# Performance work log

Measured on AMD Instinct MI355X. Metric: run time of the kernel, lower is better.

Reference implementation:

```python
import jax, jax.numpy as jnp
import numpy as np

THETA = 10000.0
NUM_HEADS = 16
MAX_SEQ_LEN = 2048

def _rope_tables(d_k, max_seq_len, theta=THETA):
    dims = jnp.arange(0, d_k, 2, dtype=jnp.float32)
    freqs = 1.0 / theta ** (dims / d_k)
    t = jnp.arange(max_seq_len, dtype=jnp.float32)
    angles = jnp.outer(t, freqs)  # (max_seq_len, d_k//2)
    return jnp.cos(angles), jnp.sin(angles)

def _apply_rope(x, token_positions, cos_tab, sin_tab):
    # x: (..., seq_len, d_k)
    cos = jnp.repeat(cos_tab[token_positions], 2, axis=-1)  # (seq_len, d_k)
    sin = jnp.repeat(sin_tab[token_positions], 2, axis=-1)
    # interleaved rotate-half: (-x1, x0, -x3, x2, ...)
    xp = x.reshape(*x.shape[:-1], -1, 2)
    x_neg = jnp.stack([-xp[..., 1], xp[..., 0]], axis=-1).reshape(x.shape)
    return x * cos + x_neg * sin

def setup_inputs() -> dict:
    key = jax.random.key(0)
    ks = jax.random.split(key, 5)
    B, S, D = 4, 2048, 1024
    scale = 1.0 / np.sqrt(D)
    return {
        "x": jax.random.normal(ks[0], (B, S, D), dtype=jnp.float32),
        "q_proj": jax.random.normal(ks[1], (D, D), dtype=jnp.float32) * scale,
        "k_proj": jax.random.normal(ks[2], (D, D), dtype=jnp.float32) * scale,
        "v_proj": jax.random.normal(ks[3], (D, D), dtype=jnp.float32) * scale,
        "o_proj": jax.random.normal(ks[4], (D, D), dtype=jnp.float32) * scale,
        "token_positions": jnp.arange(S, dtype=jnp.int64),
    }

def reference(x, q_proj, k_proj, v_proj, o_proj, token_positions):
    B, S, D = x.shape
    H = NUM_HEADS
    d_k = D // H
    cos_tab, sin_tab = _rope_tables(d_k, MAX_SEQ_LEN)

    q = (x @ q_proj).reshape(B, S, H, d_k).transpose(0, 2, 1, 3)  # (B,H,S,d_k)
    k = (x @ k_proj).reshape(B, S, H, d_k).transpose(0, 2, 1, 3)
    v = (x @ v_proj).reshape(B, S, H, d_k).transpose(0, 2, 1, 3)

    q = _apply_rope(q, token_positions, cos_tab, sin_tab)
    k = _apply_rope(k, token_positions, cos_tab, sin_tab)

    scores = jnp.einsum('bhqd,bhkd->bhqk', q, k) / jnp.sqrt(jnp.float32(d_k))
    causal = jnp.tril(jnp.ones((S, S), dtype=bool))
    scores = jnp.where(causal, scores, -jnp.inf)
    attn = jax.nn.softmax(scores, axis=-1)
    out = jnp.einsum('bhqk,bhkd->bhqd', attn, v)  # (B,H,S,d_k)
    out = out.transpose(0, 2, 1, 3).reshape(B, S, D)
    return out @ o_proj
```

## Files before the change

### kernel.cpp

```cpp
#include <hip/hip_runtime.h>
#include <hip/hip_bf16.h>
#include <stdint.h>


typedef __attribute__((ext_vector_type(8))) short short8;
typedef __attribute__((ext_vector_type(4))) float floatx4;
typedef __attribute__((ext_vector_type(16))) float floatx16;

#define MFMA16(a,b,c) __builtin_amdgcn_mfma_f32_16x16x32_bf16((a),(b),(c),0,0,0)
#define MFMA32(a,b,c) __builtin_amdgcn_mfma_f32_32x32x16_bf16((a),(b),(c),0,0,0)
#define BAR() __builtin_amdgcn_s_barrier()
#define LGKM0 asm volatile("s_waitcnt lgkmcnt(0)" ::: "memory")
#define VMCNT6 asm volatile("s_waitcnt vmcnt(6)" ::: "memory")
#define VMCNT8 asm volatile("s_waitcnt vmcnt(8)" ::: "memory")

__device__ __forceinline__ uint32_t fbits(float f){ uint32_t u; __builtin_memcpy(&u,&f,4); return u; }
__device__ __forceinline__ unsigned short f2bf(float f) {
    uint32_t u = fbits(f);
    return (unsigned short)((u + 0x7fffu + ((u>>16)&1u)) >> 16);
}
__device__ __forceinline__ float bf2f(unsigned short s){ uint32_t u = (uint32_t)s<<16; float f; __builtin_memcpy(&f,&u,4); return f; }
__device__ __forceinline__ uint32_t pkbf(float lo, float hi) {
#if __has_builtin(__builtin_amdgcn_cvt_pk_bf16_f32)
    auto r = __builtin_amdgcn_cvt_pk_bf16_f32(lo, hi);
    uint32_t u; __builtin_memcpy(&u, &r, sizeof(u));
    return u;
#else
    return __builtin_amdgcn_perm(fbits(hi)+0x8000u, fbits(lo)+0x8000u, 0x07060302u);
#endif
}
__device__ __forceinline__ float fexp2(float x) {
#if __has_builtin(__builtin_amdgcn_exp2f)
    return __builtin_amdgcn_exp2f(x);
#else
    return exp2f(x);
#endif
}

__device__ __forceinline__ void load_lds16(const unsigned short* g, unsigned short* l) {
    __builtin_amdgcn_global_load_lds(
        (const __attribute__((address_space(1))) void*)g,
        (__attribute__((address_space(3))) void*)l, 16, 0, 0);
}

__device__ __forceinline__ bool sniff_f32(const unsigned short* xr) {
    int lane = threadIdx.x & 63;
    int bad = 0;
#pragma unroll
    for (int i = 0; i < 16; i++) {
        float v = bf2f(xr[lane * 16 + i]);
        if (!(__builtin_fabsf(v) < 1e10f)) bad = 1;
    }
    return __ballot(bad != 0) != 0ull;
}

__global__ __launch_bounds__(256) void prep_k(
    const void* __restrict__ x,
    const void* __restrict__ wq, const void* __restrict__ wk,
    const void* __restrict__ wv, const void* __restrict__ wo,
    unsigned short* __restrict__ WT, unsigned short* __restrict__ WoT,
    float2* __restrict__ tab, unsigned short* __restrict__ xb) {
    int blk = blockIdx.x, t = threadIdx.x;
    bool f32 = sniff_f32((const unsigned short*)x);
    if (blk < 4096) {
        __shared__ unsigned short tile[32][33];
        int mat = blk >> 10, r = blk & 1023;
        const void* src = (mat == 0) ? wq : (mat == 1) ? wk : (mat == 2) ? wv : wo;
        unsigned short* dst = (mat < 3) ? (WT + (size_t)mat * 1048576) : WoT;
        int bx = (r & 31) * 32, by = (r >> 5) * 32;
        int tx = t & 31, ty = t >> 5;
#pragma unroll
        for (int j = 0; j < 32; j += 8) {
            size_t idx = (size_t)(by + ty + j) * 1024 + bx + tx;
            float v = f32 ? ((const float*)src)[idx] : bf2f(((const unsigned short*)src)[idx]);
            tile[ty + j][tx] = f2bf(v);
        }
        __syncthreads();
#pragma unroll
        for (int j = 0; j < 32; j += 8)
            dst[(size_t)(bx + ty + j) * 1024 + by + tx] = tile[tx][ty + j];
    } else if (blk < 4352) {
        int i = (blk - 4096) * 256 + t;
        int pos = i >> 5, j = i & 31;
        float freq = exp2f(-(float)(2 * j) * (1.0f / 64.0f) * 13.287712379549449f);
        float a = (float)pos * freq;
        tab[i] = make_float2(cosf(a), sinf(a));
    } else {
        size_t base = (size_t)(blk - 4352) * 2048 + (size_t)t * 8;
        if (f32) {
            const float4* s4 = (const float4*)((const float*)x + base);
            float4 a = s4[0], b = s4[1];
            uint4 o;
            o.x = pkbf(a.x, a.y); o.y = pkbf(a.z, a.w);
            o.z = pkbf(b.x, b.y); o.w = pkbf(b.z, b.w);
            *(uint4*)(xb + base) = o;
        } else {
            *(uint4*)(xb + base) = *(const uint4*)((const unsigned short*)x + base);
        }
    }
}

template <int MODE>
__global__ __launch_bounds__(256, 2) void gemmt(
    const unsigned short* __restrict__ A,
    const unsigned short* __restrict__ Bt,
    void* __restrict__ C0,
    unsigned short* __restrict__ C1,
    unsigned short* __restrict__ C2,
    const float2* __restrict__ tab,
    const unsigned short* __restrict__ xsniff) {
    const int K = 1024;
    extern __shared__ __align__(16) char smraw[];
    unsigned short* SL = (unsigned short*)smraw;

    int t = threadIdx.x;
    int lane = t & 63, w = t >> 6;
    int quad = lane >> 4, l15 = lane & 15;
    int wn = w * 64;

    int nbx = gridDim.x;
    int flat = blockIdx.y * nbx + blockIdx.x;
    int cpx = (nbx * gridDim.y) >> 3;
    int swzid = (flat & 7) * cpx + (flat >> 3);
    int bx = swzid % nbx, by = swzid / nbx;
    int m0 = by * 128, n0 = bx * 256;

    floatx4 acc[8][4];
#pragma unroll
    for (int i = 0; i < 8; i++)
#pragma unroll
        for (int j = 0; j < 4; j++) acc[i][j] = (floatx4){0.f, 0.f, 0.f, 0.f};

    int sg = ((t & 3) ^ ((t >> 3) & 3)) * 8;
    const unsigned short* gA = A + (size_t)(m0 + (t >> 2)) * K + sg;
    const unsigned short* gB = Bt + (size_t)(n0 + (t >> 2)) * K + sg;

    int colsw = (quad ^ ((l15 >> 1) & 3)) * 8;

#pragma unroll
    for (int kt = 0; kt < 2; kt++) {
        unsigned short* Sb = SL + kt * 12288 + w * 512;
        load_lds16(gA + kt * 32, Sb);
        load_lds16(gA + (size_t)64 * K + kt * 32, Sb + 2048);
        load_lds16(gB + kt * 32, Sb + 4096);
        load_lds16(gB + (size_t)64 * K + kt * 32, Sb + 6144);
        load_lds16(gB + (size_t)128 * K + kt * 32, Sb + 8192);
        load_lds16(gB + (size_t)192 * K + kt * 32, Sb + 10240);
    }
    VMCNT6;
    __syncthreads();

    int cur = 0, nxt = 2;
#pragma unroll 1
    for (int kt = 0; kt < 32; kt++) {
        const unsigned short* cA = SL + cur * 12288;
        const unsigned short* cB = SL + cur * 12288 + 4096;
        unsigned short* Sb = SL + nxt * 12288 + w * 512;
        int kc = (kt < 30) ? (kt + 2) : 31;
        size_t ko = (size_t)kc * 32;
        short8 af[4], bf[4];

#pragma unroll
        for (int m = 0; m < 4; m++)
            af[m] = *(const short8*)(cA + (m * 16 + l15) * 32 + colsw);
#pragma unroll
        for (int n = 0; n < 4; n++)
            bf[n] = *(const short8*)(cB + (wn + n * 16 + l15) * 32 + colsw);
        load_lds16(gA + ko, Sb);
        load_lds16(gA + (size_t)64 * K + ko, Sb + 2048);
        load_lds16(gB + ko, Sb + 4096);
        BAR(); LGKM0;
        __builtin_amdgcn_s_setprio(1);
#pragma unroll
        for (int m = 0; m < 4; m++)
#pragma unroll
            for (int n = 0; n < 4; n++) acc[m][n] = MFMA16(af[m], bf[n], acc[m][n]);
        __builtin_amdgcn_s_setprio(0);
        BAR();

#pragma unroll
        for (int m = 0; m < 4; m++)
            af[m] = *(const short8*)(cA + ((m + 4) * 16 + l15) * 32 + colsw);
        load_lds16(gB + (size_t)64 * K + ko, Sb + 6144);
        load_lds16(gB + (size_t)128 * K + ko, Sb + 8192);
        load_lds16(gB + (size_t)192 * K + ko, Sb + 10240);
        BAR(); LGKM0;
        __builtin_amdgcn_s_setprio(1);
#pragma unroll
        for (int m = 0; m < 4; m++)
#pragma unroll
            for (int n = 0; n < 4; n++) acc[m + 4][n] = MFMA16(af[m], bf[n], acc[m + 4][n]);
        __builtin_amdgcn_s_setprio(0);
        VMCNT6;
        BAR();

        cur = (cur == 2) ? 0 : cur + 1;
        nxt = (nxt == 2) ? 0 : nxt + 1;
    }

#pragma unroll
    for (int i = 0; i < 8; i++) {
#pragma unroll
        for (int j = 0; j < 4; j++) {
            int col = n0 + wn + j * 16 + l15;
            int row0 = m0 + i * 16 + quad * 4;
            int which = col >> 10, nn = col & 1023;
            int b = row0 >> 11, s0 = row0 & 2047;
            if (which == 2) {
                int hh = nn >> 6, d = nn & 63;
                uint32_t lo = pkbf(acc[i][j][0], acc[i][j][1]);
                uint32_t hi = pkbf(acc[i][j][2], acc[i][j][3]);
                *(uint64_t*)(C2 + ((size_t)((b * 16 + hh) * 64 + d)) * 2048 + s0) =
                    (uint64_t)lo | ((uint64_t)hi << 32);
            } else {
                int d = nn & 63;
                unsigned short* dst = (which == 0) ? (unsigned short*)C0 : C1;
                float sc = (which == 0) ? 0.18033688011112042f : 1.0f;
#pragma unroll
                for (int r = 0; r < 4; r++) {
                    int s = s0 + r;
                    float v = acc[i][j][r];
                    float pv = __shfl_xor(v, 1);
                    float2 cs = tab[(s << 5) + (d >> 1)];
                    float o = (d & 1) ? (v * cs.x + pv * cs.y) : (v * cs.x - pv * cs.y);
                    dst[((size_t)(b * 2048 + s)) * 1024 + nn] = f2bf(o * sc);
                }
            }
        }
    }
}

__global__ __launch_bounds__(128, 2) void gemmo(
    const unsigned short* __restrict__ A,
    const unsigned short* __restrict__ Bt,
    void* __restrict__ C0,
    const unsigned short* __restrict__ xsniff) {
    const int K = 1024;
    extern __shared__ __align__(16) char smraw[];
    unsigned short* SL = (unsigned short*)smraw;

    int t = threadIdx.x;
    int lane = t & 63, w = t >> 6;
    int quad = lane >> 4, l15 = lane & 15;
    int wn = w * 64;

    int nbx = gridDim.x;
    int flat = blockIdx.y * nbx + blockIdx.x;
    int cpx = (nbx * gridDim.y) >> 3;
    int swzid = (flat & 7) * cpx + (flat >> 3);
    int bx = swzid % nbx, by = swzid / nbx;
    int m0 = by * 128, n0 = bx * 128;

    floatx4 acc[8][4];
#pragma unroll
    for (int i = 0; i < 8; i++)
#pragma unroll
        for (int j = 0; j < 4; j++) acc[i][j] = (floatx4){0.f, 0.f, 0.f, 0.f};

    int sg = ((t & 3) ^ ((t >> 3) & 3)) * 8;
    const unsigned short* gA = A + (size_t)(m0 + (t >> 2)) * K + sg;
    const unsigned short* gB = Bt + (size_t)(n0 + (t >> 2)) * K + sg;

    int colsw = (quad ^ ((l15 >> 1) & 3)) * 8;

#pragma unroll
    for (int kt = 0; kt < 2; kt++) {
        unsigned short* Sb = SL + kt * 8192 + w * 512;
#pragma unroll
        for (int c = 0; c < 4; c++) {
            load_lds16(gA + (size_t)(c * 32) * K + kt * 32, Sb + c * 1024);
            load_lds16(gB + (size_t)(c * 32) * K + kt * 32, Sb + 4096 + c * 1024);
        }
    }
    VMCNT8;
    __syncthreads();

    int cur = 0, nxt = 2;
#pragma unroll 1
    for (int kt = 0; kt < 32; kt++) {
        const unsigned short* cA = SL + cur * 8192;
        const unsigned short* cB = SL + cur * 8192 + 4096;
        unsigned short* Sb = SL + nxt * 8192 + w * 512;
        int kc = (kt < 30) ? (kt + 2) : 31;
        size_t ko = (size_t)kc * 32;
        short8 af[4], bf[4];

#pragma unroll
        for (int m = 0; m < 4; m++)
            af[m] = *(const short8*)(cA + (m * 16 + l15) * 32 + colsw);
#pragma unroll
        for (int n = 0; n < 4; n++)
            bf[n] = *(const short8*)(cB + (wn + n * 16 + l15) * 32 + colsw);
#pragma unroll
        for (int c = 0; c < 4; c++)
            load_lds16(gA + (size_t)(c * 32) * K + ko, Sb + c * 1024);
        BAR(); LGKM0;
        __builtin_amdgcn_s_setprio(1);
#pragma unroll
        for (int m = 0; m < 4; m++)
#pragma unroll
            for (int n = 0; n < 4; n++) acc[m][n] = MFMA16(af[m], bf[n], acc[m][n]);
        __builtin_amdgcn_s_setprio(0);
        BAR();

#pragma unroll
        for (int m = 0; m < 4; m++)
            af[m] = *(const short8*)(cA + ((m + 4) * 16 + l15) * 32 + colsw);
#pragma unroll
        for (int c = 0; c < 4; c++)
            load_lds16(gB + (size_t)(c * 32) * K + ko, Sb + 4096 + c * 1024);
        BAR(); LGKM0;
        __builtin_amdgcn_s_setprio(1);
#pragma unroll
        for (int m = 0; m < 4; m++)
#pragma unroll
            for (int n = 0; n < 4; n++) acc[m + 4][n] = MFMA16(af[m], bf[n], acc[m + 4][n]);
        __builtin_amdgcn_s_setprio(0);
        VMCNT8;
        BAR();

        cur = (cur == 2) ? 0 : cur + 1;
        nxt = (nxt == 2) ? 0 : nxt + 1;
    }

    bool out_f32 = sniff_f32(xsniff);
#pragma unroll
    for (int i = 0; i < 8; i++) {
#pragma unroll
        for (int j = 0; j < 4; j++) {
            int col = n0 + wn + j * 16 + l15;
            int row0 = m0 + i * 16 + quad * 4;
#pragma unroll
            for (int r = 0; r < 4; r++) {
                size_t idx = (size_t)(row0 + r) * 1024 + col;
                if (out_f32) ((float*)C0)[idx] = acc[i][j][r];
                else ((unsigned short*)C0)[idx] = f2bf(acc[i][j][r]);
            }
        }
    }
}

__global__ __launch_bounds__(512, 4) void flash_k(
    const unsigned short* __restrict__ Qb,
    const unsigned short* __restrict__ Kb,
    const unsigned short* __restrict__ Vt,
    unsigned short* __restrict__ A2) {
    __shared__ __align__(16) unsigned short Kl[2][128 * 64];
    __shared__ __align__(16) unsigned short Vl[2][64 * 128];

    int bh = blockIdx.x;
    int y = blockIdx.y;
    int qt = (y < 4) ? (7 - y) : (y - 4);
    int b = bh >> 4, h = bh & 15;
    int t = threadIdx.x, lane = t & 63, w = t >> 6;
    int l31 = lane & 31, half = lane >> 5;
    size_t base = ((size_t)b * 2048) * 1024 + h * 64;
    int q0w = qt * 256 + w * 32;

    short8 Qf[4];
#pragma unroll
    for (int ks = 0; ks < 4; ks++)
        Qf[ks] = *(const short8*)(Qb + base + (size_t)(q0w + l31) * 1024 + ks * 16 + half * 8);

    floatx16 O[2];
    O[0] = (floatx16)0.0f; O[1] = (floatx16)0.0f;
    float lsum = 0.f;

    int nk = 2 * (qt + 1);

    int srow = t >> 3, gs = t & 7;
    const unsigned short* kg = Kb + base + (size_t)srow * 1024 + gs * 8;
    const unsigned short* vg = Vt + ((size_t)(bh * 64 + srow)) * 2048 + gs * 8;
    int kw0 = srow * 64 + ((gs ^ (srow & 7)) * 8);
    int vw0 = srow * 128 + ((gs ^ (srow & 7)) * 8);

    short8 rk0 = *(const short8*)(kg);
    short8 rk1 = *(const short8*)(kg + (size_t)64 * 1024);
    short8 rv0 = *(const short8*)(vg);
    short8 rv1 = *(const short8*)(vg + 64);

    for (int kt = 0; kt < nk; kt++) {
        int k0 = kt * 128, bf = kt & 1;
        *(short8*)&Kl[bf][kw0] = rk0;
        *(short8*)&Kl[bf][kw0 + 4096] = rk1;
        *(short8*)&Vl[bf][vw0] = rv0;
        *(short8*)&Vl[bf][vw0 + 64] = rv1;
        __syncthreads();
        if (kt + 1 < nk) {
            size_t ko2 = (size_t)(kt + 1) * 128;
            rk0 = *(const short8*)(kg + ko2 * 1024);
            rk1 = *(const short8*)(kg + (ko2 + 64) * 1024);
            rv0 = *(const short8*)(vg + ko2);
            rv1 = *(const short8*)(vg + ko2 + 64);
        }
#pragma unroll
        for (int mb = 0; mb < 4; mb++) {
            int k0mb = k0 + mb * 32;
            if (k0mb >= q0w + 32) continue;
            short8 Ka[4];
#pragma unroll
            for (int ks = 0; ks < 4; ks++)
                Ka[ks] = *(const short8*)&Kl[bf][(mb * 32 + l31) * 64 +
                                                 (((ks * 2 + half) ^ (l31 & 7)) * 8)];
            floatx16 Sc = (floatx16)0.0f;
#pragma unroll
            for (int ks = 0; ks < 4; ks++)
                Sc = MFMA32(Ka[ks], Qf[ks], Sc);

            bool domask = (k0mb + 31 > q0w);
            int thr = q0w + l31 - k0mb - half * 4;
            float p[16];
#pragma unroll
            for (int e = 0; e < 16; e++) {
                float v = fexp2(Sc[e]);
                if (domask) {
                    const int ce = (e & 3) + ((e >> 2) << 3);
                    v = (ce > thr) ? 0.f : v;
                }
                p[e] = v;
            }
            float t0 = (p[0] + p[1]) + (p[2] + p[3]);
            float t1 = (p[4] + p[5]) + (p[6] + p[7]);
            float t2 = (p[8] + p[9]) + (p[10] + p[11]);
            float t3 = (p[12] + p[13]) + (p[14] + p[15]);
            lsum += (t0 + t1) + (t2 + t3);
            uint32_t pkm[8];
#pragma unroll
            for (int jj = 0; jj < 8; jj++)
                pkm[jj] = pkbf(p[2 * jj], p[2 * jj + 1]);

            short8 Va[2][2];
#pragma unroll
            for (int db = 0; db < 2; db++)
#pragma unroll
                for (int ks2 = 0; ks2 < 2; ks2++)
                    Va[db][ks2] = *(const short8*)&Vl[bf][(db * 32 + l31) * 128 +
                                                         ((((mb * 2 + ks2) * 2 + half) ^ (l31 & 7)) * 8)];
#pragma unroll
            for (int ks2 = 0; ks2 < 2; ks2++) {
                uint32_t p0 = pkm[4 * ks2 + 0];
                uint32_t p1 = pkm[4 * ks2 + 1];
                uint32_t p2 = pkm[4 * ks2 + 2];
                uint32_t p3 = pkm[4 * ks2 + 3];
                uint32_t u = half ? p0 : p2;
                uint32_t v2 = half ? p1 : p3;
                uint32_t ya = (uint32_t)__shfl_xor((int)u, 32);
                uint32_t yb = (uint32_t)__shfl_xor((int)v2, 32);
                union { short8 s; uint32_t q[4]; } bb;
                bb.q[0] = half ? ya : p0;
                bb.q[1] = half ? yb : p1;
                bb.q[2] = half ? p2 : ya;
                bb.q[3] = half ? p3 : yb;
#pragma unroll
                for (int db = 0; db < 2; db++)
                    O[db] = MFMA32(Va[db][ks2], bb.s, O[db]);
            }
        }
    }

    float tot = lsum + __shfl_xor(lsum, 32);
    float inv = 1.0f / tot;
    int scol = q0w + l31;
    unsigned short* op = A2 + base + (size_t)scol * 1024;
#pragma unroll
    for (int db = 0; db < 2; db++) {
#pragma unroll
        for (int g = 0; g < 4; g++) {
            int d0 = db * 32 + half * 4 + g * 8;
            float v0 = O[db][g * 4 + 0] * inv;
            float v1 = O[db][g * 4 + 1] * inv;
            float v2 = O[db][g * 4 + 2] * inv;
            float v3 = O[db][g * 4 + 3] * inv;
            uint32_t lo = pkbf(v0, v1), hi = pkbf(v2, v3);
            *(uint64_t*)(op + d0) = (uint64_t)lo | ((uint64_t)hi << 32);
        }
    }
}

extern "C" void kernel_launch(void* const* d_in, const int* in_sizes, int n_in,
                              void* d_out, int out_size, void* d_ws, size_t ws_size,
                              hipStream_t stream) {
    const void* x  = d_in[0];
    const void* wq = d_in[1];
    const void* wk = d_in[2];
    const void* wv = d_in[3];
    const void* wo = d_in[4];

    char* ws = (char*)d_ws;
    unsigned short* WT  = (unsigned short*)(ws);
    unsigned short* WoT = (unsigned short*)(ws + 6291456);
    float2*         tab = (float2*)(ws + 8388608);
    unsigned short* xb  = (unsigned short*)(ws + 8913920);
    unsigned short* Qb  = (unsigned short*)(ws + 8913920 + 16777216ull);
    unsigned short* Kb  = (unsigned short*)(ws + 8913920 + 2ull * 16777216);
    unsigned short* Vt  = (unsigned short*)(ws + 8913920 + 3ull * 16777216);
    unsigned short* A2  = xb;

    (void)hipFuncSetAttribute(reinterpret_cast<const void*>(gemmt<1>),
                              hipFuncAttributeMaxDynamicSharedMemorySize, 73728);
    (void)hipFuncSetAttribute(reinterpret_cast<const void*>(gemmo),
                              hipFuncAttributeMaxDynamicSharedMemorySize, 49152);

    prep_k<<<8448, 256, 0, stream>>>(x, wq, wk, wv, wo, WT, WoT, tab, xb);

    gemmt<1><<<dim3(12, 64), 256, 73728, stream>>>(xb, WT, Qb, Kb, Vt, tab,
                                                   (const unsigned short*)x);
    flash_k<<<dim3(64, 8), 512, 0, stream>>>(Qb, Kb, Vt, A2);
    gemmo<<<dim3(8, 64), 128, 49152, stream>>>(A2, WoT, d_out,
                                               (const unsigned short*)x);
}
```

Baseline: 254.7 us.

## Use 4-wave output GEMM, shrink flash K/V tiles to 64, add MODE epilogue

The output projection GEMM goes from 2 waves to 4 waves per 128x128 tile, each wave computing a 64x64 quadrant, so each thread issues fewer loads and holds fewer accumulators. The flash attention kernel shrinks its K/V tile from 128 to 64 keys, halving LDS use and register prefetch but doubling the number of loop iterations and barriers. The QKV GEMM epilogue gains a MODE==0 plain-store path, which is inactive because the kernel is launched with MODE=1. The changes trade fewer registers and more occupancy against more sync overhead per key.

```diff
diff --git a/kernel.cpp b/kernel.cpp
--- a/kernel.cpp
+++ b/kernel.cpp
@@ -11,8 +11,8 @@
 #define MFMA32(a,b,c) __builtin_amdgcn_mfma_f32_32x32x16_bf16((a),(b),(c),0,0,0)
 #define BAR() __builtin_amdgcn_s_barrier()
 #define LGKM0 asm volatile("s_waitcnt lgkmcnt(0)" ::: "memory")
+#define VMCNT4 asm volatile("s_waitcnt vmcnt(4)" ::: "memory")
 #define VMCNT6 asm volatile("s_waitcnt vmcnt(6)" ::: "memory")
-#define VMCNT8 asm volatile("s_waitcnt vmcnt(8)" ::: "memory")
 
 __device__ __forceinline__ uint32_t fbits(float f){ uint32_t u; __builtin_memcpy(&u,&f,4); return u; }
 __device__ __forceinline__ unsigned short f2bf(float f) {
@@ -198,39 +198,49 @@
         nxt = (nxt == 2) ? 0 : nxt + 1;
     }
 
+    bool out_f32 = (MODE == 0) ? sniff_f32(xsniff) : false;
 #pragma unroll
     for (int i = 0; i < 8; i++) {
 #pragma unroll
         for (int j = 0; j < 4; j++) {
             int col = n0 + wn + j * 16 + l15;
             int row0 = m0 + i * 16 + quad * 4;
-            int which = col >> 10, nn = col & 1023;
-            int b = row0 >> 11, s0 = row0 & 2047;
-            if (which == 2) {
-                int hh = nn >> 6, d = nn & 63;
-                uint32_t lo = pkbf(acc[i][j][0], acc[i][j][1]);
-                uint32_t hi = pkbf(acc[i][j][2], acc[i][j][3]);
-                *(uint64_t*)(C2 + ((size_t)((b * 16 + hh) * 64 + d)) * 2048 + s0) =
-                    (uint64_t)lo | ((uint64_t)hi << 32);
+            if (MODE == 0) {
+#pragma unroll
+                for (int r = 0; r < 4; r++) {
+                    size_t idx = (size_t)(row0 + r) * 1024 + col;
+                    if (out_f32) ((float*)C0)[idx] = acc[i][j][r];
+                    else ((unsigned short*)C0)[idx] = f2bf(acc[i][j][r]);
+                }
             } else {
-                int d = nn & 63;
-                unsigned short* dst = (which == 0) ? (unsigned short*)C0 : C1;
-                float sc = (which == 0) ? 0.18033688011112042f : 1.0f;
-#pragma unroll
-                for (int r = 0; r < 4; r++) {
-                    int s = s0 + r;
-                    float v = acc[i][j][r];
-                    float pv = __shfl_xor(v, 1);
-                    float2 cs = tab[(s << 5) + (d >> 1)];
-                    float o = (d & 1) ? (v * cs.x + pv * cs.y) : (v * cs.x - pv * cs.y);
-                    dst[((size_t)(b * 2048 + s)) * 1024 + nn] = f2bf(o * sc);
+                int which = col >> 10, nn = col & 1023;
+                int b = row0 >> 11, s0 = row0 & 2047;
+                if (which == 2) {
+                    int hh = nn >> 6, d = nn & 63;
+                    uint32_t lo = pkbf(acc[i][j][0], acc[i][j][1]);
+                    uint32_t hi = pkbf(acc[i][j][2], acc[i][j][3]);
+                    *(uint64_t*)(C2 + ((size_t)((b * 16 + hh) * 64 + d)) * 2048 + s0) =
+                        (uint64_t)lo | ((uint64_t)hi << 32);
+                } else {
+                    int d = nn & 63;
+                    unsigned short* dst = (which == 0) ? (unsigned short*)C0 : C1;
+                    float sc = (which == 0) ? 0.18033688011112042f : 1.0f;
+#pragma unroll
+                    for (int r = 0; r < 4; r++) {
+                        int s = s0 + r;
+                        float v = acc[i][j][r];
+                        float pv = __shfl_xor(v, 1);
+                        float2 cs = tab[(s << 5) + (d >> 1)];
+                        float o = (d & 1) ? (v * cs.x + pv * cs.y) : (v * cs.x - pv * cs.y);
+                        dst[((size_t)(b * 2048 + s)) * 1024 + nn] = f2bf(o * sc);
+                    }
                 }
             }
         }
     }
 }
 
-__global__ __launch_bounds__(128, 2) void gemmo(
+__global__ __launch_bounds__(256, 2) void gemmo4(
     const unsigned short* __restrict__ A,
     const unsigned short* __restrict__ Bt,
     void* __restrict__ C0,
@@ -242,7 +252,7 @@
     int t = threadIdx.x;
     int lane = t & 63, w = t >> 6;
     int quad = lane >> 4, l15 = lane & 15;
-    int wn = w * 64;
+    int wm = (w >> 1) * 64, wn = (w & 1) * 64;
 
     int nbx = gridDim.x;
     int flat = blockIdx.y * nbx + blockIdx.x;
@@ -251,9 +261,9 @@
     int bx = swzid % nbx, by = swzid / nbx;
     int m0 = by * 128, n0 = bx * 128;
 
-    floatx4 acc[8][4];
-#pragma unroll
-    for (int i = 0; i < 8; i++)
+    floatx4 acc[4][4];
+#pragma unroll
+    for (int i = 0; i < 4; i++)
 #pragma unroll
         for (int j = 0; j < 4; j++) acc[i][j] = (floatx4){0.f, 0.f, 0.f, 0.f};
 
@@ -266,13 +276,12 @@
 #pragma unroll
     for (int kt = 0; kt < 2; kt++) {
         unsigned short* Sb = SL + kt * 8192 + w * 512;
-#pragma unroll
-        for (int c = 0; c < 4; c++) {
-            load_lds16(gA + (size_t)(c * 32) * K + kt * 32, Sb + c * 1024);
-            load_lds16(gB + (size_t)(c * 32) * K + kt * 32, Sb + 4096 + c * 1024);
-        }
-    }
-    VMCNT8;
+        load_lds16(gA + kt * 32, Sb);
+        load_lds16(gA + (size_t)64 * K + kt * 32, Sb + 2048);
+        load_lds16(gB + kt * 32, Sb + 4096);
+        load_lds16(gB + (size_t)64 * K + kt * 32, Sb + 6144);
+    }
+    VMCNT4;
     __syncthreads();
 
     int cur = 0, nxt = 2;
@@ -283,40 +292,38 @@
         unsigned short* Sb = SL + nxt * 8192 + w * 512;
         int kc = (kt < 30) ? (kt + 2) : 31;
         size_t ko = (size_t)kc * 32;
-        short8 af[4], bf[4];
-
-#pragma unroll
-        for (int m = 0; m < 4; m++)
-            af[m] = *(const short8*)(cA + (m * 16 + l15) * 32 + colsw);
+        short8 af[2], bf[4];
+
+#pragma unroll
+        for (int m = 0; m < 2; m++)
+            af[m] = *(const short8*)(cA + ((wm + m * 16 + l15)) * 32 + colsw);
 #pragma unroll
         for (int n = 0; n < 4; n++)
-            bf[n] = *(const short8*)(cB + (wn + n * 16 + l15) * 32 + colsw);
-#pragma unroll
-        for (int c = 0; c < 4; c++)
-            load_lds16(gA + (size_t)(c * 32) * K + ko, Sb + c * 1024);
+            bf[n] = *(const short8*)(cB + ((wn + n * 16 + l15)) * 32 + colsw);
+        load_lds16(gA + ko, Sb);
+        load_lds16(gA + (size_t)64 * K + ko, Sb + 2048);
         BAR(); LGKM0;
         __builtin_amdgcn_s_setprio(1);
 #pragma unroll
-        for (int m = 0; m < 4; m++)
+        for (int m = 0; m < 2; m++)
 #pragma unroll
             for (int n = 0; n < 4; n++) acc[m][n] = MFMA16(af[m], bf[n], acc[m][n]);
         __builtin_amdgcn_s_setprio(0);
         BAR();
 
 #pragma unroll
-        for (int m = 0; m < 4; m++)
-            af[m] = *(const short8*)(cA + ((m + 4) * 16 + l15) * 32 + colsw);
-#pragma unroll
-        for (int c = 0; c < 4; c++)
-            load_lds16(gB + (size_t)(c * 32) * K + ko, Sb + 4096 + c * 1024);
+        for (int m = 0; m < 2; m++)
+            af[m] = *(const short8*)(cA + ((wm + (m + 2) * 16 + l15)) * 32 + colsw);
+        load_lds16(gB + ko, Sb + 4096);
+        load_lds16(gB + (size_t)64 * K + ko, Sb + 6144);
         BAR(); LGKM0;
         __builtin_amdgcn_s_setprio(1);
 #pragma unroll
-        for (int m = 0; m < 4; m++)
-#pragma unroll
-            for (int n = 0; n < 4; n++) acc[m + 4][n] = MFMA16(af[m], bf[n], acc[m + 4][n]);
+        for (int m = 0; m < 2; m++)
+#pragma unroll
+            for (int n = 0; n < 4; n++) acc[m + 2][n] = MFMA16(af[m], bf[n], acc[m + 2][n]);
         __builtin_amdgcn_s_setprio(0);
-        VMCNT8;
+        VMCNT4;
         BAR();
 
         cur = (cur == 2) ? 0 : cur + 1;
@@ -325,11 +332,11 @@
 
     bool out_f32 = sniff_f32(xsniff);
 #pragma unroll
-    for (int i = 0; i < 8; i++) {
+    for (int i = 0; i < 4; i++) {
 #pragma unroll
         for (int j = 0; j < 4; j++) {
             int col = n0 + wn + j * 16 + l15;
-            int row0 = m0 + i * 16 + quad * 4;
+            int row0 = m0 + wm + i * 16 + quad * 4;
 #pragma unroll
             for (int r = 0; r < 4; r++) {
                 size_t idx = (size_t)(row0 + r) * 1024 + col;
@@ -345,8 +352,8 @@
     const unsigned short* __restrict__ Kb,
     const unsigned short* __restrict__ Vt,
     unsigned short* __restrict__ A2) {
-    __shared__ __align__(16) unsigned short Kl[2][128 * 64];
-    __shared__ __align__(16) unsigned short Vl[2][64 * 128];
+    __shared__ __align__(16) unsigned short Kl[2][64 * 64];
+    __shared__ __align__(16) unsigned short Vl[2][64 * 64];
 
     int bh = blockIdx.x;
     int y = blockIdx.y;
@@ -366,35 +373,28 @@
     O[0] = (floatx16)0.0f; O[1] = (floatx16)0.0f;
     float lsum = 0.f;
 
-    int nk = 2 * (qt + 1);
+    int nk = 4 * (qt + 1);
 
     int srow = t >> 3, gs = t & 7;
     const unsigned short* kg = Kb + base + (size_t)srow * 1024 + gs * 8;
     const unsigned short* vg = Vt + ((size_t)(bh * 64 + srow)) * 2048 + gs * 8;
-    int kw0 = srow * 64 + ((gs ^ (srow & 7)) * 8);
-    int vw0 = srow * 128 + ((gs ^ (srow & 7)) * 8);
-
-    short8 rk0 = *(const short8*)(kg);
-    short8 rk1 = *(const short8*)(kg + (size_t)64 * 1024);
-    short8 rv0 = *(const short8*)(vg);
-    short8 rv1 = *(const short8*)(vg + 64);
+    int sw = srow * 64 + ((gs ^ (srow & 7)) * 8);
+
+    short8 rk = *(const short8*)(kg);
+    short8 rv = *(const short8*)(vg);
 
     for (int kt = 0; kt < nk; kt++) {
-        int k0 = kt * 128, bf = kt & 1;
-        *(short8*)&Kl[bf][kw0] = rk0;
-        *(short8*)&Kl[bf][kw0 + 4096] = rk1;
-        *(short8*)&Vl[bf][vw0] = rv0;
-        *(short8*)&Vl[bf][vw0 + 64] = rv1;
+        int k0 = kt * 64, bf = kt & 1;
+        *(short8*)&Kl[bf][sw] = rk;
+        *(short8*)&Vl[bf][sw] = rv;
         __syncthreads();
         if (kt + 1 < nk) {
-            size_t ko2 = (size_t)(kt + 1) * 128;
-            rk0 = *(const short8*)(kg + ko2 * 1024);
-            rk1 = *(const short8*)(kg + (ko2 + 64) * 1024);
-            rv0 = *(const short8*)(vg + ko2);
-            rv1 = *(const short8*)(vg + ko2 + 64);
-        }
-#pragma unroll
-        for (int mb = 0; mb < 4; mb++) {
+            size_t ko = (size_t)(kt + 1) * 64;
+            rk = *(const short8*)(kg + ko * 1024);
+            rv = *(const short8*)(vg + ko);
+        }
+#pragma unroll
+        for (int mb = 0; mb < 2; mb++) {
             int k0mb = k0 + mb * 32;
             if (k0mb >= q0w + 32) continue;
             short8 Ka[4];
@@ -434,7 +434,7 @@
             for (int db = 0; db < 2; db++)
 #pragma unroll
                 for (int ks2 = 0; ks2 < 2; ks2++)
-                    Va[db][ks2] = *(const short8*)&Vl[bf][(db * 32 + l31) * 128 +
+                    Va[db][ks2] = *(const short8*)&Vl[bf][(db * 32 + l31) * 64 +
                                                          ((((mb * 2 + ks2) * 2 + half) ^ (l31 & 7)) * 8)];
 #pragma unroll
             for (int ks2 = 0; ks2 < 2; ks2++) {
@@ -498,7 +498,7 @@
 
     (void)hipFuncSetAttribute(reinterpret_cast<const void*>(gemmt<1>),
                               hipFuncAttributeMaxDynamicSharedMemorySize, 73728);
-    (void)hipFuncSetAttribute(reinterpret_cast<const void*>(gemmo),
+    (void)hipFuncSetAttribute(reinterpret_cast<const void*>(gemmo4),
                               hipFuncAttributeMaxDynamicSharedMemorySize, 49152);
 
     prep_k<<<8448, 256, 0, stream>>>(x, wq, wk, wv, wo, WT, WoT, tab, xb);
@@ -506,6 +506,6 @@
     gemmt<1><<<dim3(12, 64), 256, 73728, stream>>>(xb, WT, Qb, Kb, Vt, tab,
                                                    (const unsigned short*)x);
     flash_k<<<dim3(64, 8), 512, 0, stream>>>(Qb, Kb, Vt, A2);
-    gemmo<<<dim3(8, 64), 128, 49152, stream>>>(A2, WoT, d_out,
-                                               (const unsigned short*)x);
-}
+    gemmo4<<<dim3(8, 64), 256, 49152, stream>>>(A2, WoT, d_out,
+                                                (const unsigned short*)x);
+}
```

New measurement: 246.9 us. 1.03x faster.
